# Optimization experiments

Hardware: AMD Instinct MI355X
Metric: run time of the kernel (lower is better)

## Reference

```python
import jax, jax.numpy as jnp
import numpy as np

B, T, L = 512, 1024, 48


def setup_inputs() -> dict:
    key = jax.random.key(0)
    k_e, k_tr, k_st, k_en = jax.random.split(key, 4)
    emissions = jax.random.normal(k_e, (B, T, L), dtype=jnp.float32)
    mask = jnp.ones((B, T), dtype=bool)  # unused by the original decode body
    transitions = jax.random.normal(k_tr, (L, L), dtype=jnp.float32) * 0.1
    start_transitions = jax.random.normal(k_st, (L,), dtype=jnp.float32) * 0.1
    end_transitions = jax.random.normal(k_en, (L,), dtype=jnp.float32) * 0.1
    return {
        "emissions": emissions,
        "mask": mask,
        "transitions": transitions,
        "start_transitions": start_transitions,
        "end_transitions": end_transitions,
    }


def reference(emissions, mask, transitions, start_transitions, end_transitions):
    # Viterbi forward (max-plus recurrence) over time, vectorized over batch.
    v0 = start_transitions[None, :] + emissions[:, 0]  # [B, L]

    def step(v, e_t):
        # scores[b, i, j] = v[b, i] + transitions[i, j]
        scores = v[:, :, None] + transitions[None, :, :]  # [B, L, L]
        best = jnp.max(scores, axis=1)                    # [B, L]
        bp = jnp.argmax(scores, axis=1).astype(jnp.int32)  # [B, L] best prev tag
        return best + e_t, bp

    em_rest = jnp.moveaxis(emissions[:, 1:], 1, 0)  # [T-1, B, L]
    v_final, bps = jax.lax.scan(step, v0, em_rest)  # bps: [T-1, B, L]
    v_final = v_final + end_transitions[None, :]
    best_last = jnp.argmax(v_final, axis=1).astype(jnp.int32)  # [B]

    # Backtrack: bps[t] maps tag at time t+1 -> best tag at time t.
    def back(tag, bp):
        prev = jnp.take_along_axis(bp, tag[:, None], axis=1)[:, 0]  # [B]
        return prev, prev

    _, tags_0_to_Tm2 = jax.lax.scan(back, best_last, bps, reverse=True)  # [T-1, B]
    paths = jnp.concatenate([tags_0_to_Tm2, best_last[None, :]], axis=0)  # [T, B]
    return paths.T  # [B, T] decoded tag sequences
```

## Files before the change

kernel.cpp:

```cpp
#include <hip/hip_runtime.h>
#include <math.h>

#define BB 512
#define TT 1024
#define LL 48
#define PF 8
#define TSTRIDE 49

__device__ __forceinline__ float readlane_f(float v, int lane) {
    return __int_as_float(__builtin_amdgcn_readlane(__float_as_int(v), lane));
}

template <int CTRL>
__device__ __forceinline__ float dppmax(float x) {
    int y = __builtin_amdgcn_update_dpp(__float_as_int(x), __float_as_int(x),
                                        CTRL, 0xF, 0xF, false);
    return fmaxf(x, __int_as_float(y));
}

__device__ __forceinline__ int wave_argmax(float z) {
    float r = z;
    r = dppmax<0xB1>(r);
    r = dppmax<0x4E>(r);
    r = dppmax<0x141>(r);
    r = dppmax<0x140>(r);
    r = dppmax<0x142>(r);
    r = dppmax<0x143>(r);
    float m = readlane_f(r, 63);
    unsigned long long eq = __ballot(z == m);
    return (int)__builtin_ctzll(eq);
}

__global__ __launch_bounds__(64)
__attribute__((amdgpu_waves_per_eu(1, 1)))
void viterbi_kernel(
    const float* __restrict__ emissions,
    const float* __restrict__ transitions,
    const float* __restrict__ start_tr,
    const float* __restrict__ end_tr,
    int* __restrict__ out,
    float* __restrict__ vws)
{
    __shared__ float tlds[LL * TSTRIDE];

    const int b  = blockIdx.x;
    const int j  = threadIdx.x;
    const int jc = (j < LL) ? j : (LL - 1);

    float tc[LL];
#pragma unroll
    for (int i = 0; i < LL; ++i) {
        tc[i] = transitions[i * LL + jc];
        tlds[i * TSTRIDE + jc] = tc[i];
    }
#pragma unroll
    for (int i = 0; i < LL; ++i)
        asm volatile("" : "+v"(tc[i]));

    const float* em = emissions + (size_t)b * TT * LL;
    float* vr_g = vws + (size_t)b * TT * LL;

    float v = start_tr[jc] + em[jc];
    vr_g[jc] = v;

    float er[PF];
#pragma unroll
    for (int k = 0; k < PF; ++k)
        er[k] = em[(size_t)(1 + k) * LL + jc];

    auto step = [&](int t, float e) {
        float s[LL];
#pragma unroll
        for (int i = 0; i < LL; ++i)
            s[i] = readlane_f(v, i) + tc[i];

        float m1[16];
#pragma unroll
        for (int k = 0; k < 16; ++k)
            m1[k] = fmaxf(fmaxf(s[3 * k], s[3 * k + 1]), s[3 * k + 2]);
        float m2[6];
#pragma unroll
        for (int k = 0; k < 5; ++k)
            m2[k] = fmaxf(fmaxf(m1[3 * k], m1[3 * k + 1]), m1[3 * k + 2]);
        m2[5] = m1[15];
        float best = fmaxf(fmaxf(fmaxf(m2[0], m2[1]), m2[2]),
                           fmaxf(fmaxf(m2[3], m2[4]), m2[5]));

        v = best + e;
        vr_g[(size_t)t * LL + jc] = v;
    };

    int tb = 1;
    for (; tb + PF <= TT; tb += PF) {
#pragma unroll
        for (int k = 0; k < PF; ++k) {
            int t = tb + k;
            float e = er[k];
            int tn = t + PF; if (tn > TT - 1) tn = TT - 1;
            er[k] = em[(size_t)tn * LL + jc];
            step(t, e);
        }
    }
#pragma unroll
    for (int k = 0; k < PF - 1; ++k) {
        int t = tb + k;
        if (t < TT) step(t, er[k]);
    }

    float vf = (j < LL) ? (v + end_tr[jc]) : -INFINITY;
    int tag = wave_argmax(vf);

    int* ob = out + (size_t)b * TT;
    if (j == 0) ob[TT - 1] = tag;

    for (int hi = TT - 2; hi >= 0; hi -= 32) {
        int lo = hi - 31; if (lo < 0) lo = 0;
        int n = hi - lo + 1;

        float vr[32];
#pragma unroll
        for (int k = 31; k >= 0; --k)
            if (k < n) vr[k] = vr_g[(size_t)(lo + k) * LL + jc];

        int outv = 0;
#pragma unroll
        for (int k = 31; k >= 0; --k) {
            if (k < n) {
                float tcol = tlds[jc * TSTRIDE + tag];
                float z = (j < LL) ? (vr[k] + tcol) : -INFINITY;
                tag = wave_argmax(z);
                outv = (j == k) ? tag : outv;
            }
        }
        if (j < n) ob[lo + j] = outv;
    }
}

extern "C" void kernel_launch(void* const* d_in, const int* in_sizes, int n_in,
                              void* d_out, int out_size, void* d_ws, size_t ws_size,
                              hipStream_t stream) {
    const float* emissions   = (const float*)d_in[0];
    const float* transitions = (const float*)d_in[2];
    const float* start_tr    = (const float*)d_in[3];
    const float* end_tr      = (const float*)d_in[4];
    int* out = (int*)d_out;

    float* vws = (float*)d_ws;

    viterbi_kernel<<<dim3(BB), dim3(64), 0, stream>>>(
        emissions, transitions, start_tr, end_tr, out, vws);
}
```

Baseline: 542.7 us.

## Process two batch rows per wave and broadcast Viterbi scores through LDS

Each 64-thread block now decodes two batch sequences together, interleaving their forward max-plus recurrences and their backtracking argmax chains to expose instruction-level parallelism across independent dependency chains. The per-step broadcast of the previous score vector moves from 48 scalar readlanes to a volatile LDS write followed by float4 LDS reads. The grid is halved, which leaves each CU with a single wave and doubles the serial work per wave. That trade only pays off if the two interleaved chains hide each other's latency.

```diff
diff --git a/kernel.cpp b/kernel.cpp
--- a/kernel.cpp
+++ b/kernel.cpp
@@ -31,6 +31,39 @@
     return (int)__builtin_ctzll(eq);
 }
 
+__device__ __attribute__((always_inline)) void step2(
+    float& vA, float& vB, const float* __restrict__ tc,
+    const float* vbufA, const float* vbufB,
+    volatile float* wA, volatile float* wB,
+    float eA, float eB)
+{
+    *wA = vA;
+    *wB = vB;
+    float pmA[12], pmB[12];
+#pragma unroll
+    for (int r = 0; r < 12; ++r) {
+        float4 qA, qB;
+        __builtin_memcpy(&qA, &vbufA[4 * r], 16);
+        __builtin_memcpy(&qB, &vbufB[4 * r], 16);
+        float a0 = qA.x + tc[4 * r + 0], b0 = qB.x + tc[4 * r + 0];
+        float a1 = qA.y + tc[4 * r + 1], b1 = qB.y + tc[4 * r + 1];
+        float a2 = qA.z + tc[4 * r + 2], b2 = qB.z + tc[4 * r + 2];
+        float a3 = qA.w + tc[4 * r + 3], b3 = qB.w + tc[4 * r + 3];
+        pmA[r] = fmaxf(fmaxf(a0, a1), fmaxf(a2, a3));
+        pmB[r] = fmaxf(fmaxf(b0, b1), fmaxf(b2, b3));
+    }
+    float cA0 = fmaxf(fmaxf(pmA[0], pmA[1]), pmA[2]);
+    float cB0 = fmaxf(fmaxf(pmB[0], pmB[1]), pmB[2]);
+    float cA1 = fmaxf(fmaxf(pmA[3], pmA[4]), pmA[5]);
+    float cB1 = fmaxf(fmaxf(pmB[3], pmB[4]), pmB[5]);
+    float cA2 = fmaxf(fmaxf(pmA[6], pmA[7]), pmA[8]);
+    float cB2 = fmaxf(fmaxf(pmB[6], pmB[7]), pmB[8]);
+    float cA3 = fmaxf(fmaxf(pmA[9], pmA[10]), pmA[11]);
+    float cB3 = fmaxf(fmaxf(pmB[9], pmB[10]), pmB[11]);
+    vA = fmaxf(fmaxf(cA0, cA1), fmaxf(cA2, cA3)) + eA;
+    vB = fmaxf(fmaxf(cB0, cB1), fmaxf(cB2, cB3)) + eB;
+}
+
 __global__ __launch_bounds__(64)
 __attribute__((amdgpu_waves_per_eu(1, 1)))
 void viterbi_kernel(
@@ -42,8 +75,11 @@
     float* __restrict__ vws)
 {
     __shared__ float tlds[LL * TSTRIDE];
-
-    const int b  = blockIdx.x;
+    __shared__ __align__(16) float vbufA[64];
+    __shared__ __align__(16) float vbufB[64];
+
+    const int bA = blockIdx.x * 2;
+    const int bB = bA + 1;
     const int j  = threadIdx.x;
     const int jc = (j < LL) ? j : (LL - 1);
 
@@ -57,82 +93,95 @@
     for (int i = 0; i < LL; ++i)
         asm volatile("" : "+v"(tc[i]));
 
-    const float* em = emissions + (size_t)b * TT * LL;
-    float* vr_g = vws + (size_t)b * TT * LL;
-
-    float v = start_tr[jc] + em[jc];
-    vr_g[jc] = v;
-
-    float er[PF];
-#pragma unroll
-    for (int k = 0; k < PF; ++k)
-        er[k] = em[(size_t)(1 + k) * LL + jc];
-
-    auto step = [&](int t, float e) {
-        float s[LL];
-#pragma unroll
-        for (int i = 0; i < LL; ++i)
-            s[i] = readlane_f(v, i) + tc[i];
-
-        float m1[16];
-#pragma unroll
-        for (int k = 0; k < 16; ++k)
-            m1[k] = fmaxf(fmaxf(s[3 * k], s[3 * k + 1]), s[3 * k + 2]);
-        float m2[6];
-#pragma unroll
-        for (int k = 0; k < 5; ++k)
-            m2[k] = fmaxf(fmaxf(m1[3 * k], m1[3 * k + 1]), m1[3 * k + 2]);
-        m2[5] = m1[15];
-        float best = fmaxf(fmaxf(fmaxf(m2[0], m2[1]), m2[2]),
-                           fmaxf(fmaxf(m2[3], m2[4]), m2[5]));
-
-        v = best + e;
-        vr_g[(size_t)t * LL + jc] = v;
-    };
+    const float* emA = emissions + (size_t)bA * TT * LL;
+    const float* emB = emissions + (size_t)bB * TT * LL;
+    float* vgA = vws + (size_t)bA * TT * LL;
+    float* vgB = vws + (size_t)bB * TT * LL;
+
+    float vA = start_tr[jc] + emA[jc];
+    float vB = start_tr[jc] + emB[jc];
+    vgA[jc] = vA;
+    vgB[jc] = vB;
+
+    float erA[PF], erB[PF];
+#pragma unroll
+    for (int k = 0; k < PF; ++k) {
+        erA[k] = emA[(size_t)(1 + k) * LL + jc];
+        erB[k] = emB[(size_t)(1 + k) * LL + jc];
+    }
+
+    volatile float* wA = &vbufA[j];
+    volatile float* wB = &vbufB[j];
 
     int tb = 1;
     for (; tb + PF <= TT; tb += PF) {
 #pragma unroll
         for (int k = 0; k < PF; ++k) {
             int t = tb + k;
-            float e = er[k];
+            float eA = erA[k];
+            float eB = erB[k];
             int tn = t + PF; if (tn > TT - 1) tn = TT - 1;
-            er[k] = em[(size_t)tn * LL + jc];
-            step(t, e);
+            erA[k] = emA[(size_t)tn * LL + jc];
+            erB[k] = emB[(size_t)tn * LL + jc];
+            step2(vA, vB, tc, vbufA, vbufB, wA, wB, eA, eB);
+            vgA[(size_t)t * LL + jc] = vA;
+            vgB[(size_t)t * LL + jc] = vB;
         }
     }
 #pragma unroll
     for (int k = 0; k < PF - 1; ++k) {
         int t = tb + k;
-        if (t < TT) step(t, er[k]);
-    }
-
-    float vf = (j < LL) ? (v + end_tr[jc]) : -INFINITY;
-    int tag = wave_argmax(vf);
-
-    int* ob = out + (size_t)b * TT;
-    if (j == 0) ob[TT - 1] = tag;
+        if (t < TT) {
+            step2(vA, vB, tc, vbufA, vbufB, wA, wB, erA[k], erB[k]);
+            vgA[(size_t)t * LL + jc] = vA;
+            vgB[(size_t)t * LL + jc] = vB;
+        }
+    }
+
+    float et = end_tr[jc];
+    float vfA = (j < LL) ? (vA + et) : -INFINITY;
+    float vfB = (j < LL) ? (vB + et) : -INFINITY;
+    int tagA = wave_argmax(vfA);
+    int tagB = wave_argmax(vfB);
+
+    int* obA = out + (size_t)bA * TT;
+    int* obB = out + (size_t)bB * TT;
+    if (j == 0) {
+        obA[TT - 1] = tagA;
+        obB[TT - 1] = tagB;
+    }
 
     for (int hi = TT - 2; hi >= 0; hi -= 32) {
         int lo = hi - 31; if (lo < 0) lo = 0;
         int n = hi - lo + 1;
 
-        float vr[32];
-#pragma unroll
-        for (int k = 31; k >= 0; --k)
-            if (k < n) vr[k] = vr_g[(size_t)(lo + k) * LL + jc];
-
-        int outv = 0;
+        float vrA[32], vrB[32];
 #pragma unroll
         for (int k = 31; k >= 0; --k) {
             if (k < n) {
-                float tcol = tlds[jc * TSTRIDE + tag];
-                float z = (j < LL) ? (vr[k] + tcol) : -INFINITY;
-                tag = wave_argmax(z);
-                outv = (j == k) ? tag : outv;
+                vrA[k] = vgA[(size_t)(lo + k) * LL + jc];
+                vrB[k] = vgB[(size_t)(lo + k) * LL + jc];
             }
         }
-        if (j < n) ob[lo + j] = outv;
+
+        int outA = 0, outB = 0;
+#pragma unroll
+        for (int k = 31; k >= 0; --k) {
+            if (k < n) {
+                float tcA = tlds[jc * TSTRIDE + tagA];
+                float tcB = tlds[jc * TSTRIDE + tagB];
+                float zA = (j < LL) ? (vrA[k] + tcA) : -INFINITY;
+                float zB = (j < LL) ? (vrB[k] + tcB) : -INFINITY;
+                tagA = wave_argmax(zA);
+                tagB = wave_argmax(zB);
+                outA = (j == k) ? tagA : outA;
+                outB = (j == k) ? tagB : outB;
+            }
+        }
+        if (j < n) {
+            obA[lo + j] = outA;
+            obB[lo + j] = outB;
+        }
     }
 }
 
@@ -147,6 +196,6 @@
 
     float* vws = (float*)d_ws;
 
-    viterbi_kernel<<<dim3(BB), dim3(64), 0, stream>>>(
+    viterbi_kernel<<<dim3(BB / 2), dim3(64), 0, stream>>>(
         emissions, transitions, start_tr, end_tr, out, vws);
 }
```

Result: slower. 1.133 ms (+108.8%).

## Replace per-step readlane broadcast with DPP butterfly and permlane-swap max reduction

Applied to the files above, without the earlier changes.

The forward max-plus step no longer broadcasts all 48 previous scores through scalar readlanes. Each lane now collects the 16 scores of its row with a DPP butterfly and adds four precomputed transition sets, one per 16-lane row. The four partial maxima are then combined across rows with v_permlane16/32_swap. This is meant to cut the serial readlane latency on the recurrence's critical path. In exchange it does more VALU work and holds more transition registers, which adds register pressure.

```diff
diff --git a/kernel.cpp b/kernel.cpp
--- a/kernel.cpp
+++ b/kernel.cpp
@@ -12,10 +12,26 @@
 }
 
 template <int CTRL>
+__device__ __forceinline__ unsigned dppu(unsigned x) {
+    return (unsigned)__builtin_amdgcn_update_dpp((int)x, (int)x, CTRL, 0xF, 0xF, false);
+}
+
+template <int CTRL>
 __device__ __forceinline__ float dppmax(float x) {
     int y = __builtin_amdgcn_update_dpp(__float_as_int(x), __float_as_int(x),
                                         CTRL, 0xF, 0xF, false);
     return fmaxf(x, __int_as_float(y));
+}
+
+__device__ __forceinline__ void pl16_swap2(unsigned& a, unsigned& b, unsigned x) {
+    a = x;
+    asm("v_mov_b32 %0, %1" : "=&v"(b) : "v"(a));
+    asm("v_permlane16_swap_b32 %0, %1" : "+v"(a), "+v"(b));
+}
+__device__ __forceinline__ void pl32_swap2(unsigned& a, unsigned& b, unsigned x) {
+    a = x;
+    asm("v_mov_b32 %0, %1" : "=&v"(b) : "v"(a));
+    asm("v_permlane32_swap_b32 %0, %1" : "+v"(a), "+v"(b));
 }
 
 __device__ __forceinline__ int wave_argmax(float z) {
@@ -31,6 +47,26 @@
     return (int)__builtin_ctzll(eq);
 }
 
+__device__ __forceinline__ void bfly16(unsigned x, unsigned g[16]) {
+    g[0] = x;
+    g[1] = dppu<0xB1>(g[0]);
+    g[2] = dppu<0x4E>(g[0]);
+    g[3] = dppu<0x4E>(g[1]);
+#pragma unroll
+    for (int p = 0; p < 4; ++p) g[4 + p] = dppu<0x141>(g[p]);
+#pragma unroll
+    for (int p = 0; p < 8; ++p) g[8 + p] = dppu<0x140>(g[p]);
+}
+
+__device__ __forceinline__ float max16(const float s[16]) {
+    float m0 = fmaxf(fmaxf(s[0], s[1]), s[2]);
+    float m1 = fmaxf(fmaxf(s[3], s[4]), s[5]);
+    float m2 = fmaxf(fmaxf(s[6], s[7]), s[8]);
+    float m3 = fmaxf(fmaxf(s[9], s[10]), s[11]);
+    float m4 = fmaxf(fmaxf(s[12], s[13]), s[14]);
+    return fmaxf(fmaxf(fmaxf(m0, m1), fmaxf(m2, m3)), fmaxf(m4, s[15]));
+}
+
 __global__ __launch_bounds__(64)
 __attribute__((amdgpu_waves_per_eu(1, 1)))
 void viterbi_kernel(
@@ -47,15 +83,43 @@
     const int j  = threadIdx.x;
     const int jc = (j < LL) ? j : (LL - 1);
 
-    float tc[LL];
-#pragma unroll
-    for (int i = 0; i < LL; ++i) {
-        tc[i] = transitions[i * LL + jc];
-        tlds[i * TSTRIDE + jc] = tc[i];
-    }
 #pragma unroll
     for (int i = 0; i < LL; ++i)
-        asm volatile("" : "+v"(tc[i]));
+        tlds[i * TSTRIDE + jc] = transitions[i * LL + jc];
+
+    unsigned gi[16];
+    bfly16((unsigned)j, gi);
+#pragma unroll
+    for (int p = 0; p < 16; ++p) asm("" : "+v"(gi[p]));
+
+    unsigned ca, cb;
+    pl16_swap2(ca, cb, (unsigned)j);
+    const bool useA16 = (ca == (unsigned)(j ^ 16));
+    unsigned da, db;
+    pl32_swap2(da, db, (unsigned)j);
+    const bool useA32 = (da == (unsigned)(j ^ 32));
+
+    const int d0 = jc;
+    const int d1 = min(j ^ 16, LL - 1);
+    const int d2 = min(j ^ 32, LL - 1);
+    const int d3 = min(j ^ 48, LL - 1);
+    float tcp0[16], tcp1[16], tcp2[16], tcp3[16];
+#pragma unroll
+    for (int p = 0; p < 16; ++p) {
+        const int src = min((int)gi[p], LL - 1);
+        const float* trow = transitions + src * LL;
+        tcp0[p] = trow[d0];
+        tcp1[p] = trow[d1];
+        tcp2[p] = trow[d2];
+        tcp3[p] = trow[d3];
+    }
+#pragma unroll
+    for (int p = 0; p < 16; ++p) {
+        asm("" : "+v"(tcp0[p]));
+        asm("" : "+v"(tcp1[p]));
+        asm("" : "+v"(tcp2[p]));
+        asm("" : "+v"(tcp3[p]));
+    }
 
     const float* em = emissions + (size_t)b * TT * LL;
     float* vr_g = vws + (size_t)b * TT * LL;
@@ -69,24 +133,34 @@
         er[k] = em[(size_t)(1 + k) * LL + jc];
 
     auto step = [&](int t, float e) {
-        float s[LL];
-#pragma unroll
-        for (int i = 0; i < LL; ++i)
-            s[i] = readlane_f(v, i) + tc[i];
-
-        float m1[16];
-#pragma unroll
-        for (int k = 0; k < 16; ++k)
-            m1[k] = fmaxf(fmaxf(s[3 * k], s[3 * k + 1]), s[3 * k + 2]);
-        float m2[6];
-#pragma unroll
-        for (int k = 0; k < 5; ++k)
-            m2[k] = fmaxf(fmaxf(m1[3 * k], m1[3 * k + 1]), m1[3 * k + 2]);
-        m2[5] = m1[15];
-        float best = fmaxf(fmaxf(fmaxf(m2[0], m2[1]), m2[2]),
-                           fmaxf(fmaxf(m2[3], m2[4]), m2[5]));
-
-        v = best + e;
+        unsigned g[16];
+        bfly16(__float_as_uint(v), g);
+
+        float s[16];
+#pragma unroll
+        for (int p = 0; p < 16; ++p) s[p] = __uint_as_float(g[p]) + tcp0[p];
+        const float P0 = max16(s);
+#pragma unroll
+        for (int p = 0; p < 16; ++p) s[p] = __uint_as_float(g[p]) + tcp1[p];
+        const float P1 = max16(s);
+#pragma unroll
+        for (int p = 0; p < 16; ++p) s[p] = __uint_as_float(g[p]) + tcp2[p];
+        const float P2 = max16(s);
+#pragma unroll
+        for (int p = 0; p < 16; ++p) s[p] = __uint_as_float(g[p]) + tcp3[p];
+        const float P3 = max16(s);
+
+        unsigned a1, b1; pl16_swap2(a1, b1, __float_as_uint(P1));
+        const float r1 = useA16 ? __uint_as_float(a1) : __uint_as_float(b1);
+        unsigned a3, b3; pl16_swap2(a3, b3, __float_as_uint(P3));
+        const float r3 = useA16 ? __uint_as_float(a3) : __uint_as_float(b3);
+        const float Q0 = fmaxf(P0, r1);
+        const float Q2 = fmaxf(P2, r3);
+
+        unsigned a2, b2; pl32_swap2(a2, b2, __float_as_uint(Q2));
+        const float r2 = useA32 ? __uint_as_float(a2) : __uint_as_float(b2);
+
+        v = fmaxf(Q0, r2) + e;
         vr_g[(size_t)t * LL + jc] = v;
     };
 
```

Result: slower. 578.5 us (+6.6%).
